# Optimization experiments

Hardware: AMD Instinct MI355X
Metric: run time of the kernel (lower is better)

Reference implementation:

```python
import jax, jax.numpy as jnp
import numpy as np

N = 100000   # nodes
E = 1600000  # directed edges (before self-loops)
D_IN, D_HID, D_OUT = 128, 128, 16


def _glorot(key, shape):
    lim = np.sqrt(6.0 / (shape[0] + shape[1])).astype(np.float32)
    return jax.random.uniform(key, shape, jnp.float32, -lim, lim)


def setup_inputs() -> dict:
    key = jax.random.key(0)
    ks = jax.random.split(key, 5)
    x = jax.random.normal(ks[0], (N, D_IN), jnp.float32)
    edge_index = jax.random.randint(ks[1], (2, E), 0, N, dtype=jnp.int32)
    return {
        "x": x,
        "edge_index": edge_index,
        "W1": _glorot(ks[2], (D_IN, D_HID)),
        "b1": jnp.zeros((D_HID,), jnp.float32),
        "W2": _glorot(ks[3], (D_HID, D_HID)),
        "b2": jnp.zeros((D_HID,), jnp.float32),
        "W3": _glorot(ks[4], (D_HID, D_OUT)),
        "b3": jnp.zeros((D_OUT,), jnp.float32),
    }


def _gcn_conv(x, W, b, src, dst, norm):
    # GCNConv: linear transform, then normalized sum-aggregation into dst, then bias.
    h = x @ W                                    # [N, Dout]
    msg = h[src] * norm[:, None]                 # [E+N, Dout] gathered messages
    return jax.ops.segment_sum(msg, dst, num_segments=N) + b


def reference(x, edge_index, W1, b1, W2, b2, W3, b3):
    # add self-loops (PyG GCNConv default add_self_loops=True)
    loops = jnp.arange(N, dtype=edge_index.dtype)
    src = jnp.concatenate([edge_index[0], loops])
    dst = jnp.concatenate([edge_index[1], loops])
    # symmetric normalization D^{-1/2} (A+I) D^{-1/2}; degree over destinations
    deg = jax.ops.segment_sum(jnp.ones_like(dst, jnp.float32), dst, num_segments=N)
    dis = jnp.where(deg > 0, jax.lax.rsqrt(jnp.maximum(deg, 1.0)), 0.0)
    norm = dis[src] * dis[dst]

    h = jax.nn.relu(_gcn_conv(x, W1, b1, src, dst, norm))   # dropout is identity in eval mode
    h = jax.nn.relu(_gcn_conv(h, W2, b2, src, dst, norm))
    return _gcn_conv(h, W3, b3, src, dst, norm)
```

## Files before the change

kernel.cpp:

```cpp
#include <hip/hip_runtime.h>

#define NN 100000
#define EE 1600000
#define DH 128
#define DO 16
#define NBLK1 98

__global__ __launch_bounds__(256) void k_zero(int* __restrict__ meta) {
    int v = blockIdx.x * 256 + threadIdx.x;
    if (v < NN) meta[v] = 0;
}

__global__ __launch_bounds__(256) void k_hist(const int* __restrict__ dst,
                                              int* __restrict__ meta) {
    int e = blockIdx.x * 256 + threadIdx.x;
    if (e < EE) atomicAdd(meta + dst[e], 1);
}

__global__ __launch_bounds__(1024) void k_scan1(int* __restrict__ meta,
                                                int* __restrict__ bsum) {
    __shared__ int sm[1024];
    const int t = threadIdx.x;
    const int idx = blockIdx.x * 1024 + t;
    int c = (idx < NN) ? meta[idx] : 0;
    int v = c;
    sm[t] = v;
    __syncthreads();
    for (int off = 1; off < 1024; off <<= 1) {
        int add = (t >= off) ? sm[t - off] : 0;
        __syncthreads();
        v += add;
        sm[t] = v;
        __syncthreads();
    }
    if (t == 1023) bsum[blockIdx.x] = v;
    if (idx < NN) meta[idx] = v - c;
}

__global__ __launch_bounds__(128) void k_scan2(int* __restrict__ bsum) {
    __shared__ int sm[128];
    const int t = threadIdx.x;
    int c = (t < NBLK1) ? bsum[t] : 0;
    int v = c;
    sm[t] = v;
    __syncthreads();
    for (int off = 1; off < 128; off <<= 1) {
        int add = (t >= off) ? sm[t - off] : 0;
        __syncthreads();
        v += add;
        sm[t] = v;
        __syncthreads();
    }
    if (t < NBLK1) bsum[t] = v - c;
}

__global__ __launch_bounds__(256) void k_scan3(int* __restrict__ meta,
                                               const int* __restrict__ bsum) {
    int idx = blockIdx.x * 256 + threadIdx.x;
    if (idx < NN) meta[idx] += bsum[idx >> 10];
}

__global__ __launch_bounds__(256) void k_scatter(const int* __restrict__ ei,
                                                 int* __restrict__ meta,
                                                 int* __restrict__ cs) {
    int e = blockIdx.x * 256 + threadIdx.x;
    if (e < EE) {
        int d = ei[EE + e];
        int pos = atomicAdd(meta + d, 1);
        cs[pos] = ei[e];
    }
}

__global__ __launch_bounds__(512, 4) void k_gemm128(const float* __restrict__ in,
                                                    const float* __restrict__ W,
                                                    const int* __restrict__ meta,
                                                    float* __restrict__ out) {
    __shared__ float Wl[DH * 64];
    const int colbase = (blockIdx.x & 1) * 64;
    for (int i = threadIdx.x * 4; i < DH * 64; i += 512 * 4) {
        const int r = i >> 6;
        const int c = i & 63;
        *(float4*)(Wl + i) = *(const float4*)(W + r * DH + colbase + c);
    }
    __syncthreads();

    const int wid  = threadIdx.x >> 6;
    const int lane = threadIdx.x & 63;
    const int cp   = lane & 31;
    const int rh   = lane >> 5;
    const int c2   = cp * 2;

    const int rbw = (blockIdx.x >> 1) * 64 + wid * 8;
    if (rbw >= NN) return;

    const int r0 = rbw + rh * 4;
    const float* x0 = in + (size_t)r0 * DH;

    float2 acc0 = {0.f, 0.f}, acc1 = {0.f, 0.f};
    float2 acc2 = {0.f, 0.f}, acc3 = {0.f, 0.f};

    for (int k = 0; k < DH; k += 4) {
        const float4 a0 = *(const float4*)(x0 + 0 * DH + k);
        const float4 a1 = *(const float4*)(x0 + 1 * DH + k);
        const float4 a2 = *(const float4*)(x0 + 2 * DH + k);
        const float4 a3 = *(const float4*)(x0 + 3 * DH + k);

        const float2 w0 = *(const float2*)(Wl + (k + 0) * 64 + c2);
        const float2 w1 = *(const float2*)(Wl + (k + 1) * 64 + c2);
        const float2 w2 = *(const float2*)(Wl + (k + 2) * 64 + c2);
        const float2 w3 = *(const float2*)(Wl + (k + 3) * 64 + c2);

        acc0.x = fmaf(a0.x, w0.x, acc0.x); acc0.y = fmaf(a0.x, w0.y, acc0.y);
        acc0.x = fmaf(a0.y, w1.x, acc0.x); acc0.y = fmaf(a0.y, w1.y, acc0.y);
        acc0.x = fmaf(a0.z, w2.x, acc0.x); acc0.y = fmaf(a0.z, w2.y, acc0.y);
        acc0.x = fmaf(a0.w, w3.x, acc0.x); acc0.y = fmaf(a0.w, w3.y, acc0.y);

        acc1.x = fmaf(a1.x, w0.x, acc1.x); acc1.y = fmaf(a1.x, w0.y, acc1.y);
        acc1.x = fmaf(a1.y, w1.x, acc1.x); acc1.y = fmaf(a1.y, w1.y, acc1.y);
        acc1.x = fmaf(a1.z, w2.x, acc1.x); acc1.y = fmaf(a1.z, w2.y, acc1.y);
        acc1.x = fmaf(a1.w, w3.x, acc1.x); acc1.y = fmaf(a1.w, w3.y, acc1.y);

        acc2.x = fmaf(a2.x, w0.x, acc2.x); acc2.y = fmaf(a2.x, w0.y, acc2.y);
        acc2.x = fmaf(a2.y, w1.x, acc2.x); acc2.y = fmaf(a2.y, w1.y, acc2.y);
        acc2.x = fmaf(a2.z, w2.x, acc2.x); acc2.y = fmaf(a2.z, w2.y, acc2.y);
        acc2.x = fmaf(a2.w, w3.x, acc2.x); acc2.y = fmaf(a2.w, w3.y, acc2.y);

        acc3.x = fmaf(a3.x, w0.x, acc3.x); acc3.y = fmaf(a3.x, w0.y, acc3.y);
        acc3.x = fmaf(a3.y, w1.x, acc3.x); acc3.y = fmaf(a3.y, w1.y, acc3.y);
        acc3.x = fmaf(a3.z, w2.x, acc3.x); acc3.y = fmaf(a3.z, w2.y, acc3.y);
        acc3.x = fmaf(a3.w, w3.x, acc3.x); acc3.y = fmaf(a3.w, w3.y, acc3.y);
    }

    const int bprev = (r0 == 0) ? 0 : meta[r0 - 1];
    const int e0 = meta[r0 + 0];
    const int e1 = meta[r0 + 1];
    const int e2 = meta[r0 + 2];
    const int e3 = meta[r0 + 3];
    const float d0 = 1.0f / sqrtf((float)(e0 - bprev + 1));
    const float d1 = 1.0f / sqrtf((float)(e1 - e0 + 1));
    const float d2 = 1.0f / sqrtf((float)(e2 - e1 + 1));
    const float d3 = 1.0f / sqrtf((float)(e3 - e2 + 1));
    acc0.x *= d0; acc0.y *= d0;
    acc1.x *= d1; acc1.y *= d1;
    acc2.x *= d2; acc2.y *= d2;
    acc3.x *= d3; acc3.y *= d3;

    float* o0 = out + (size_t)r0 * DH + colbase + c2;
    *(float2*)(o0 + 0 * DH) = acc0;
    *(float2*)(o0 + 1 * DH) = acc1;
    *(float2*)(o0 + 2 * DH) = acc2;
    *(float2*)(o0 + 3 * DH) = acc3;
}

__global__ __launch_bounds__(256) void k_gemm16(const float* __restrict__ in,
                                                const float* __restrict__ W,
                                                const int* __restrict__ meta,
                                                float* __restrict__ out) {
    __shared__ float Wl[DH * DO];
    for (int i = threadIdx.x * 4; i < DH * DO; i += 256 * 4)
        *(float4*)(Wl + i) = *(const float4*)(W + i);
    __syncthreads();

    const int lane = threadIdx.x & 63;
    const int col  = lane & 15;
    const int rsub = lane >> 4;
    const int gw   = blockIdx.x * 4 + (threadIdx.x >> 6);
    const int strd = gridDim.x * 4;

    for (int rb = gw * 4; rb < NN; rb += strd * 4) {
        int row = rb + rsub;
        const float* x0 = in + (size_t)row * DH;
        float acc = 0.f;
        for (int k = 0; k < DH; k += 4) {
            float4 a = *(const float4*)(x0 + k);
            acc = fmaf(a.x, Wl[(k + 0) * DO + col], acc);
            acc = fmaf(a.y, Wl[(k + 1) * DO + col], acc);
            acc = fmaf(a.z, Wl[(k + 2) * DO + col], acc);
            acc = fmaf(a.w, Wl[(k + 3) * DO + col], acc);
        }
        const int e  = meta[row];
        const int bg = (row == 0) ? 0 : meta[row - 1];
        const float dl = 1.0f / sqrtf((float)(e - bg + 1));
        out[(size_t)row * DO + col] = acc * dl;
    }
}

template <bool RELU_OUT>
__global__ __launch_bounds__(256) void k_agg128(const float* __restrict__ msg,
                                                const int* __restrict__ meta,
                                                const int* __restrict__ cs,
                                                const float* __restrict__ b,
                                                float* __restrict__ out) {
    const int wid  = threadIdx.x >> 6;
    const int lane = threadIdx.x & 63;
    const float2 bb = *(const float2*)(b + lane * 2);
    const int d = blockIdx.x * 4 + wid;
    if (d >= NN) return;
    const int du  = __builtin_amdgcn_readfirstlane(d);
    const int end = meta[du];
    const int beg = (du == 0) ? 0 : meta[du - 1];
    const float dd = 1.0f / sqrtf((float)(end - beg + 1));

    float2 acc = *((const float2*)(msg + (size_t)du * DH) + lane);

    int j = beg;
    for (; j + 4 <= end; j += 4) {
        int s0 = cs[j], s1 = cs[j + 1], s2 = cs[j + 2], s3 = cs[j + 3];
        float2 v0 = *((const float2*)(msg + (size_t)s0 * DH) + lane);
        float2 v1 = *((const float2*)(msg + (size_t)s1 * DH) + lane);
        float2 v2 = *((const float2*)(msg + (size_t)s2 * DH) + lane);
        float2 v3 = *((const float2*)(msg + (size_t)s3 * DH) + lane);
        acc.x += (v0.x + v1.x) + (v2.x + v3.x);
        acc.y += (v0.y + v1.y) + (v2.y + v3.y);
    }
    for (; j < end; ++j) {
        int s0 = cs[j];
        float2 v0 = *((const float2*)(msg + (size_t)s0 * DH) + lane);
        acc.x += v0.x; acc.y += v0.y;
    }
    float2 o; o.x = bb.x + dd * acc.x; o.y = bb.y + dd * acc.y;
    if (RELU_OUT) { o.x = fmaxf(o.x, 0.f); o.y = fmaxf(o.y, 0.f); }
    *((float2*)(out + (size_t)du * DH) + lane) = o;
}

__global__ __launch_bounds__(256) void k_agg16(const float* __restrict__ msg,
                                               const int* __restrict__ meta,
                                               const int* __restrict__ cs,
                                               const float* __restrict__ b,
                                               float* __restrict__ out) {
    int i = blockIdx.x * 256 + threadIdx.x;
    if (i >= NN * DO) return;
    const int v   = i >> 4;
    const int col = i & 15;
    const int end = meta[v];
    const int beg = (v == 0) ? 0 : meta[v - 1];
    const float dd = 1.0f / sqrtf((float)(end - beg + 1));

    float acc = msg[(size_t)v * DO + col];
    int j = beg;
    for (; j + 4 <= end; j += 4) {
        int s0 = cs[j], s1 = cs[j + 1], s2 = cs[j + 2], s3 = cs[j + 3];
        acc += (msg[(size_t)s0 * DO + col] + msg[(size_t)s1 * DO + col])
             + (msg[(size_t)s2 * DO + col] + msg[(size_t)s3 * DO + col]);
    }
    for (; j < end; ++j) acc += msg[(size_t)cs[j] * DO + col];
    out[i] = b[col] + dd * acc;
}

extern "C" void kernel_launch(void* const* d_in, const int* in_sizes, int n_in,
                              void* d_out, int out_size, void* d_ws, size_t ws_size,
                              hipStream_t stream) {
    (void)in_sizes; (void)n_in; (void)out_size; (void)ws_size;
    const float* x  = (const float*)d_in[0];
    const int*   ei = (const int*)d_in[1];
    const float* W1 = (const float*)d_in[2];
    const float* b1 = (const float*)d_in[3];
    const float* W2 = (const float*)d_in[4];
    const float* b2 = (const float*)d_in[5];
    const float* W3 = (const float*)d_in[6];
    const float* b3 = (const float*)d_in[7];
    float* out = (float*)d_out;

    int*   meta = (int*)d_ws;
    int*   baux = meta + NN;
    int*   cs   = baux + 128;
    float* A    = (float*)(cs + EE);
    float* B    = A + (size_t)NN * DH;
    float* C    = A;

    k_zero   <<<391, 256, 0, stream>>>(meta);
    k_hist   <<<6250, 256, 0, stream>>>(ei + EE, meta);
    k_scan1  <<<NBLK1, 1024, 0, stream>>>(meta, baux);
    k_scan2  <<<1, 128, 0, stream>>>(baux);
    k_scan3  <<<391, 256, 0, stream>>>(meta, baux);
    k_scatter<<<6250, 256, 0, stream>>>(ei, meta, cs);

    const int G128 = 1563 * 2;

    k_gemm128<<<G128, 512, 0, stream>>>(x, W1, meta, A);
    k_agg128<true><<<25000, 256, 0, stream>>>(A, meta, cs, b1, B);

    k_gemm128<<<G128, 512, 0, stream>>>(B, W2, meta, A);
    k_agg128<true><<<25000, 256, 0, stream>>>(A, meta, cs, b2, B);

    k_gemm16<<<6250, 256, 0, stream>>>(B, W3, meta, C);
    k_agg16<<<6250, 256, 0, stream>>>(C, meta, cs, b3, out);
}
```

Measured before the change: 821.7 us.

## Build CSR via two-pass bucketed partition to localize scatter atomics

Replaces the single random-scatter CSR build with a two-pass approach. Edges are first partitioned into buckets of 64 destination nodes using per-bucket atomic cursors into a staging buffer. Each bucket is then scattered by one block, so the atomics and writes stay within a small, cache-local region. This adds an extra pass over the edges and a staging buffer that aliases the feature workspace, in exchange for less random atomic traffic spread across the whole node range.

```diff
diff --git a/kernel.cpp b/kernel.cpp
--- a/kernel.cpp
+++ b/kernel.cpp
@@ -5,6 +5,8 @@
 #define DH 128
 #define DO 16
 #define NBLK1 98
+#define BSH 6
+#define NB 1563
 
 __global__ __launch_bounds__(256) void k_zero(int* __restrict__ meta) {
     int v = blockIdx.x * 256 + threadIdx.x;
@@ -60,14 +62,41 @@
     if (idx < NN) meta[idx] += bsum[idx >> 10];
 }
 
-__global__ __launch_bounds__(256) void k_scatter(const int* __restrict__ ei,
-                                                 int* __restrict__ meta,
-                                                 int* __restrict__ cs) {
+__global__ __launch_bounds__(256) void k_bstart(const int* __restrict__ meta,
+                                                int* __restrict__ bstart,
+                                                int* __restrict__ bcur) {
+    int b = blockIdx.x * 256 + threadIdx.x;
+    if (b < NB) {
+        int s = meta[b << BSH];
+        bstart[b] = s;
+        bcur[b] = s;
+    } else if (b == NB) {
+        bstart[NB] = EE;
+    }
+}
+
+__global__ __launch_bounds__(256) void kb_part(const int* __restrict__ ei,
+                                               int* __restrict__ bcur,
+                                               int2* __restrict__ stg) {
     int e = blockIdx.x * 256 + threadIdx.x;
     if (e < EE) {
+        int s = ei[e];
         int d = ei[EE + e];
-        int pos = atomicAdd(meta + d, 1);
-        cs[pos] = ei[e];
+        int pos = atomicAdd(bcur + (d >> BSH), 1);
+        stg[pos] = make_int2(s, d);
+    }
+}
+
+__global__ __launch_bounds__(256) void kb_scatter(const int2* __restrict__ stg,
+                                                  const int* __restrict__ bstart,
+                                                  int* __restrict__ meta,
+                                                  int* __restrict__ cs) {
+    const int beg = bstart[blockIdx.x];
+    const int end = bstart[blockIdx.x + 1];
+    for (int i = beg + threadIdx.x; i < end; i += 256) {
+        int2 p = stg[i];
+        int pos = atomicAdd(meta + p.y, 1);
+        cs[pos] = p.x;
     }
 }
 
@@ -267,13 +296,18 @@
     float* A    = (float*)(cs + EE);
     float* B    = A + (size_t)NN * DH;
     float* C    = A;
+    int2*  stg    = (int2*)A;
+    int*   bstart = (int*)(stg + EE);
+    int*   bcur   = bstart + NB + 1;
 
     k_zero   <<<391, 256, 0, stream>>>(meta);
     k_hist   <<<6250, 256, 0, stream>>>(ei + EE, meta);
     k_scan1  <<<NBLK1, 1024, 0, stream>>>(meta, baux);
     k_scan2  <<<1, 128, 0, stream>>>(baux);
     k_scan3  <<<391, 256, 0, stream>>>(meta, baux);
-    k_scatter<<<6250, 256, 0, stream>>>(ei, meta, cs);
+    k_bstart <<<(NB + 256) / 256, 256, 0, stream>>>(meta, bstart, bcur);
+    kb_part  <<<6250, 256, 0, stream>>>(ei, bcur, stg);
+    kb_scatter<<<NB, 256, 0, stream>>>(stg, bstart, meta, cs);
 
     const int G128 = 1563 * 2;
 
```

Result: slower. 980.3 us (+19.3%).
